# Kernel tuning notes

Measured on AMD Instinct MI355X. Metric: run time of the kernel, lower is better.

The kernel has to match this reference:

```python
import jax, jax.numpy as jnp
import numpy as np

NUM_HEAD = 2
KR = 3          # kernel_range = [3, 3]
SHIFT = 1
N_P = KR * KR   # 9 taps
PAD = (KR // 2) * SHIFT  # 1
OFFSETS = [(i, j) for i in (-(KR // 2), 0, KR // 2) if True for j in ()]  # placeholder, real list below
OFFSETS = [(i, j) for i in range(-(KR // 2), KR // 2 + 1) for j in range(-(KR // 2), KR // 2 + 1)]


def _conv3x3(x, w, b):
    # x: [B,H,W,Cin], w: [3,3,Cin,Cout] -> SAME conv + bias
    y = jax.lax.conv_general_dilated(
        x, w, window_strides=(1, 1), padding='SAME',
        dimension_numbers=('NHWC', 'HWIO', 'NHWC'))
    return y + b


def setup_inputs() -> dict:
    key = jax.random.key(0)
    B, H, W, D = 4, 128, 128, 64
    ks = jax.random.split(key, 10)
    sc = 0.05  # small init like glorot
    return {
        'x': jax.random.normal(ks[0], (B, H, W, D), jnp.float32),
        # 1x1 conv kernels stored as matrices (equiv. to (1,1,Cin,Cout))
        'K_P': jax.random.normal(ks[1], (D, D * N_P), jnp.float32) * sc,
        'V_P': jax.random.normal(ks[2], (D, D * N_P), jnp.float32) * sc,
        'Q_P': jax.random.normal(ks[3], (D, D), jnp.float32) * sc,
        'ff1_kernel': jax.random.normal(ks[4], (D, D), jnp.float32) * sc,
        'ff1_bias': jax.random.normal(ks[5], (D,), jnp.float32) * sc,
        'ff2_kernel': jax.random.normal(ks[6], (3, 3, D, 2 * D), jnp.float32) * sc,
        'ff2_bias': jax.random.normal(ks[7], (2 * D,), jnp.float32) * sc,
        'ff3_kernel': jax.random.normal(ks[8], (3, 3, 2 * D, D), jnp.float32) * sc,
        'ff3_bias': jax.random.normal(ks[9], (D,), jnp.float32) * sc,
    }


def reference(x, K_P, V_P, Q_P, ff1_kernel, ff1_bias, ff2_kernel, ff2_bias,
              ff3_kernel, ff3_bias):
    B, H, W, D = x.shape
    hd = D // NUM_HEAD

    # 1x1 projections; K/V produce N_P channel chunks, one per tap
    x_k = jnp.einsum('bhwd,de->bhwe', x, K_P).reshape(B, H, W, N_P, D)
    x_v = jnp.einsum('bhwd,de->bhwe', x, V_P).reshape(B, H, W, N_P, D)
    x_q = jnp.einsum('bhwd,de->bhwe', x, Q_P)

    pad5 = ((0, 0), (PAD, PAD), (PAD, PAD), (0, 0), (0, 0))
    k_pad = jnp.pad(x_k, pad5)
    v_pad = jnp.pad(x_v, pad5)

    # tap t uses channel chunk t at spatial offset OFFSETS[t]*SHIFT
    def taps(padded):
        return jnp.stack(
            [padded[:, PAD + i * SHIFT:PAD + i * SHIFT + H,
                    PAD + j * SHIFT:PAD + j * SHIFT + W, t, :]
             for t, (i, j) in enumerate(OFFSETS)], axis=3)  # [B,H,W,N_P,D]

    k_taps = taps(k_pad)
    v_taps = taps(v_pad)

    # validity mask (padded taps get score 0 before softmax, as in original)
    m_pad = jnp.pad(jnp.ones((B, H, W), x.dtype), ((0, 0), (PAD, PAD), (PAD, PAD)))
    mask = jnp.stack(
        [m_pad[:, PAD + i * SHIFT:PAD + i * SHIFT + H,
               PAD + j * SHIFT:PAD + j * SHIFT + W]
         for (i, j) in OFFSETS], axis=3)  # [B,H,W,N_P]

    kh = k_taps.reshape(B, H, W, N_P, NUM_HEAD, hd)
    vh = v_taps.reshape(B, H, W, N_P, NUM_HEAD, hd)
    qh = x_q.reshape(B, H, W, NUM_HEAD, hd)

    # scores per head over taps; masked-multiply then /3, as in original
    scores = jnp.einsum('bhwtnc,bhwnc->bhwnt', kh, qh)
    scores = scores * mask[:, :, :, None, :] / 3.0
    alpha = jax.nn.softmax(scores, axis=-1)  # over taps
    attn = jnp.einsum('bhwnt,bhwtnc->bhwnc', alpha, vh).reshape(B, H, W, D)

    # FFN: 1x1 conv -> relu -> 3x3 conv -> relu -> 3x3 conv -> relu
    t = jax.nn.relu(jnp.einsum('bhwd,de->bhwe', attn, ff1_kernel) + ff1_bias)
    t = jax.nn.relu(_conv3x3(t, ff2_kernel, ff2_bias))
    t = jax.nn.relu(_conv3x3(t, ff3_kernel, ff3_bias))
    return t
```

## Files before the change

### kernel.cpp

```cpp
#include <hip/hip_runtime.h>


typedef _Float16 half8 __attribute__((ext_vector_type(8)));
typedef float f32x4 __attribute__((ext_vector_type(4)));

#define PLANE 524288

__device__ __forceinline__ f32x4 mfma16(half8 a, half8 b, f32x4 c) {
  return __builtin_amdgcn_mfma_f32_16x16x32_f16(a, b, c, 0, 0, 0);
}
__device__ __forceinline__ half8 ldfrag(const _Float16* p) { return *(const half8*)p; }
__device__ __forceinline__ half8 zfrag() { half8 z = {}; return z; }

__device__ __forceinline__ void gload_lds16(const _Float16* g, _Float16* l) {
  __builtin_amdgcn_global_load_lds(
      (const __attribute__((address_space(1))) void*)g,
      (__attribute__((address_space(3))) void*)l, 16, 0, 0);
}

__global__ __launch_bounds__(256) void prep(
    const float* __restrict__ x, const float* __restrict__ Kp,
    const float* __restrict__ Vp, const float* __restrict__ Qp,
    const float* __restrict__ W1, const float* __restrict__ F2,
    const float* __restrict__ F3, _Float16* __restrict__ xh,
    _Float16* __restrict__ out) {
  if (blockIdx.x < 2048) {
    const int t = threadIdx.x;
    const int px = blockIdx.x * 32 + (t >> 3);
    const int oct = t & 7;
    const float4* s = (const float4*)(x + (size_t)px * 64 + oct * 8);
    float4 a = s[0], b = s[1];
    half8 h = { (_Float16)a.x, (_Float16)a.y, (_Float16)a.z, (_Float16)a.w,
                (_Float16)b.x, (_Float16)b.y, (_Float16)b.z, (_Float16)b.w };
    *(half8*)(xh + (size_t)oct * PLANE + (size_t)px * 8) = h;
    return;
  }
  int e = (blockIdx.x - 2048) * 256 + threadIdx.x;
  int j = e & 7, l = (e >> 3) & 63, f = e >> 9;
  int l15 = l & 15, q8 = (l >> 4) * 8;
  float v;
  if (f < 8)        { int mb = f >> 1, kb = f & 1;
                      v = Qp[(kb*32 + q8 + j) * 64 + mb*16 + l15]; }
  else if (f < 80)  { int g = f - 8, t = g >> 3, mb = (g >> 1) & 3, kb = g & 1;
                      v = Kp[(kb*32 + q8 + j) * 576 + t*64 + mb*16 + l15]; }
  else if (f < 152) { int g = f - 80, t = g >> 3, kb = (g >> 2) & 1, nb = g & 3;
                      v = Vp[(kb*32 + q8 + j) * 576 + t*64 + nb*16 + l15]; }
  else if (f < 160) { int g = f - 152, kb = g >> 2, nb = g & 3;
                      v = W1[(kb*32 + q8 + j) * 64 + nb*16 + l15]; }
  else if (f < 304) { int g = f - 160, t = g >> 4, kb = (g >> 3) & 1, nb = g & 7;
                      v = F2[(t*64 + kb*32 + q8 + j) * 128 + nb*16 + l15]; }
  else              { int g = f - 304, t = g >> 4, kb = (g >> 2) & 3, nb = g & 3;
                      v = F3[(t*128 + kb*32 + q8 + j) * 64 + nb*16 + l15]; }
  out[e] = (_Float16)v;
}

__global__ __launch_bounds__(512) void attn_ff1(
    const _Float16* __restrict__ xh, const _Float16* __restrict__ wf,
    const float* __restrict__ f1b, _Float16* __restrict__ t1g) {
  extern __shared__ _Float16 smem[];
  const int lane = threadIdx.x & 63, wid = threadIdx.x >> 6;
  const int l15 = lane & 15, q8 = (lane >> 4) * 8;
  const int row = blockIdx.x * 2 + (wid >> 2);
  const int rw = wid & 3;
  const int p0 = row * 128 + rw * 32;
  const int h = row & 127;
  const int w0 = rw * 32;
  const int oct0 = lane >> 4;
  float* dent = (float*)(smem + 77824) + wid * 64;

  {
    const _Float16* gw = wf + 4096 + (size_t)(wid * 19) * 512;
    _Float16* lw = smem + wid * 19 * 512;
    for (int i = 0; i < 19; ++i)
      gload_lds16(gw + i * 512 + lane * 8, lw + i * 512);
  }

  half8 ax0[2], ax1[2];
#pragma unroll
  for (int m = 0; m < 2; ++m) {
    const size_t px = (size_t)(p0 + m * 16 + l15);
    ax0[m] = ldfrag(xh + (size_t)oct0 * PLANE + px * 8);
    ax1[m] = ldfrag(xh + (size_t)(oct0 + 4) * PLANE + px * 8);
  }
  f32x4 qT[2][4];
#pragma unroll
  for (int cb = 0; cb < 4; ++cb) {
    half8 aq0 = ldfrag(wf + (cb * 2 + 0) * 512 + lane * 8);
    half8 aq1 = ldfrag(wf + (cb * 2 + 1) * 512 + lane * 8);
#pragma unroll
    for (int m = 0; m < 2; ++m) {
      f32x4 c = {};
      c = mfma16(aq0, ax0[m], c);
      c = mfma16(aq1, ax1[m], c);
      qT[m][cb] = c;
    }
  }

  auto load_tap = [&](int t, half8 (&x0)[2], half8 (&x1)[2]) {
    const int dh = t / 3 - 1, dw = t % 3 - 1;
    const bool rk = (unsigned)(h + dh) < 128u;
#pragma unroll
    for (int m = 0; m < 2; ++m) {
      const bool cv = rk && ((unsigned)(w0 + m * 16 + l15 + dw) < 128u);
      const size_t px = (size_t)(p0 + m * 16 + l15 + dh * 128 + dw);
      x0[m] = cv ? ldfrag(xh + (size_t)oct0 * PLANE + px * 8) : zfrag();
      x1[m] = cv ? ldfrag(xh + (size_t)(oct0 + 4) * PLANE + px * 8) : zfrag();
    }
  };

  float den0[2] = {0.f, 0.f}, den1[2] = {0.f, 0.f};
  auto score_tap = [&](int t, half8 (&x0)[2], half8 (&x1)[2],
                       float (&e0)[2], float (&e1)[2]) {
    const int dh = t / 3 - 1;
    const bool rowok = (unsigned)(h + dh) < 128u;
    half8 kf[8];
    if (rowok) {
#pragma unroll
      for (int f = 0; f < 8; ++f)
        kf[f] = ldfrag(smem + (t * 8 + f) * 512 + lane * 8);
    }
#pragma unroll
    for (int m = 0; m < 2; ++m) {
      float pa = 0.f, pb = 0.f;
      if (rowok) {
#pragma unroll
        for (int cb = 0; cb < 4; ++cb) {
          f32x4 c = {};
          c = mfma16(kf[cb * 2 + 0], x0[m], c);
          c = mfma16(kf[cb * 2 + 1], x1[m], c);
          float d = qT[m][cb].x * c.x + qT[m][cb].y * c.y
                  + qT[m][cb].z * c.z + qT[m][cb].w * c.w;
          if (cb < 2) pa += d; else pb += d;
        }
        pa += __shfl_xor(pa, 16, 64); pa += __shfl_xor(pa, 32, 64);
        pb += __shfl_xor(pb, 16, 64); pb += __shfl_xor(pb, 32, 64);
      }
      e0[m] = __expf(pa * (1.f / 3.f));
      e1[m] = __expf(pb * (1.f / 3.f));
      den0[m] += e0[m]; den1[m] += e1[m];
    }
  };

  half8 sx0[2], sx1[2];
  load_tap(0, sx0, sx1);

  __syncthreads();

  float e0c[2], e1c[2];
  score_tap(0, sx0, sx1, e0c, e1c);

  const _Float16* BVl = smem + 36864;
  f32x4 at[2][4];
#pragma unroll
  for (int m = 0; m < 2; ++m)
#pragma unroll
    for (int nb = 0; nb < 4; ++nb) at[m][nb] = f32x4{};

#pragma unroll
  for (int t = 0; t < 9; ++t) {
    const bool rowok = (unsigned)(h + (t / 3 - 1)) < 128u;
    half8 nx0[2], nx1[2];
    if (t < 8) load_tap(t + 1, nx0, nx1);
    if (rowok) {
      half8 vf[8];
#pragma unroll
      for (int f = 0; f < 8; ++f) vf[f] = ldfrag(BVl + (t * 8 + f) * 512 + lane * 8);
#pragma unroll
      for (int m = 0; m < 2; ++m) {
        _Float16 h0 = (_Float16)e0c[m], h1 = (_Float16)e1c[m];
        half8 b0 = {h0, h0, h0, h0, h0, h0, h0, h0};
        half8 b1 = {h1, h1, h1, h1, h1, h1, h1, h1};
        half8 s00 = sx0[m] * b0, s01 = sx1[m] * b0;
        half8 s10 = sx0[m] * b1, s11 = sx1[m] * b1;
#pragma unroll
        for (int nb = 0; nb < 2; ++nb) {
          at[m][nb]     = mfma16(s00, vf[0 * 4 + nb],     at[m][nb]);
          at[m][nb]     = mfma16(s01, vf[1 * 4 + nb],     at[m][nb]);
          at[m][nb + 2] = mfma16(s10, vf[0 * 4 + nb + 2], at[m][nb + 2]);
          at[m][nb + 2] = mfma16(s11, vf[1 * 4 + nb + 2], at[m][nb + 2]);
        }
      }
    }
    if (t < 8) {
      float e0n[2], e1n[2];
      score_tap(t + 1, nx0, nx1, e0n, e1n);
#pragma unroll
      for (int m = 0; m < 2; ++m) {
        sx0[m] = nx0[m]; sx1[m] = nx1[m];
        e0c[m] = e0n[m]; e1c[m] = e1n[m];
      }
    }
  }

#pragma unroll
  for (int m = 0; m < 2; ++m) {
    dent[(m * 2 + 0) * 16 + l15] = den0[m];
    dent[(m * 2 + 1) * 16 + l15] = den1[m];
  }
  f32x4 iv[2][2];
#pragma unroll
  for (int m = 0; m < 2; ++m)
#pragma unroll
    for (int hd = 0; hd < 2; ++hd) {
      f32x4 dv = *(const f32x4*)(dent + (m * 2 + hd) * 16 + (lane >> 4) * 4);
      iv[m][hd] = f32x4{1.f / dv.x, 1.f / dv.y, 1.f / dv.z, 1.f / dv.w};
    }

  __syncthreads();
  _Float16* myt = smem + wid * 2304;
#pragma unroll
  for (int m = 0; m < 2; ++m)
#pragma unroll
    for (int nb = 0; nb < 4; ++nb) {
      const int hd = nb >> 1;
#pragma unroll
      for (int r = 0; r < 4; ++r)
        myt[m * 1152 + ((lane >> 4) * 4 + r) * 72 + nb * 16 + l15] =
            (_Float16)(at[m][nb][r] * iv[m][hd][r]);
    }
  const _Float16* B1l = smem + 73728;
#pragma unroll
  for (int m = 0; m < 2; ++m) {
    half8 aa0 = ldfrag(myt + m * 1152 + l15 * 72 + q8);
    half8 aa1 = ldfrag(myt + m * 1152 + l15 * 72 + 32 + q8);
#pragma unroll
    for (int nb = 0; nb < 4; ++nb) {
      f32x4 c = {};
      c = mfma16(aa0, ldfrag(B1l + (0 * 4 + nb) * 512 + lane * 8), c);
      c = mfma16(aa1, ldfrag(B1l + (1 * 4 + nb) * 512 + lane * 8), c);
      float bv = f1b[nb * 16 + l15];
      const int ch = nb * 16 + l15;
      const size_t pbase = (size_t)(ch >> 3) * PLANE + (ch & 7);
#pragma unroll
      for (int r = 0; r < 4; ++r) {
        float v = fmaxf(c[r] + bv, 0.f);
        size_t px = (size_t)(p0 + m * 16 + (lane >> 4) * 4 + r);
        t1g[pbase + px * 8] = (_Float16)v;
      }
    }
  }
}

template <int KB, int NBL, int COUT>
__global__ __launch_bounds__(512, 2) void conv3x3(
    const _Float16* __restrict__ in, const _Float16* __restrict__ wfrag,
    const float* __restrict__ bias, void* __restrict__ outp, int out_fp32) {
  extern __shared__ _Float16 smem[];
  const int lane = threadIdx.x & 63, wid = threadIdx.x >> 6;
  const int l15 = lane & 15;
  const int nh = blockIdx.x & 1;
  const int pairIdx = blockIdx.x >> 1;
  const int row = pairIdx * 2 + (wid >> 2);
  const int rw = wid & 3;
  const int p0 = row * 128 + rw * 32;
  const int h = row & 127;
  const int w0 = rw * 32;
  const int NBF = COUT / 16;
  const int oct0 = lane >> 4;

  {
    for (int s = 0; s < 9; ++s) {
      int f = wid * 9 + s;
      int t = f >> 3, r = f & 7, kb = r / NBL, i = r % NBL;
      const _Float16* g = wfrag + (size_t)((t * KB + kb) * NBF + nh * NBL + i) * 512;
      gload_lds16(g + lane * 8, smem + f * 512);
    }
  }

  f32x4 acc[2][NBL];
#pragma unroll
  for (int m = 0; m < 2; ++m)
#pragma unroll
    for (int nb = 0; nb < NBL; ++nb) acc[m][nb] = f32x4{};

  half8 a[2][KB];
  {
    const bool rk = (unsigned)(h - 1) < 128u;
#pragma unroll
    for (int m = 0; m < 2; ++m) {
      const bool cv = rk && ((unsigned)(w0 + m * 16 + l15 - 1) < 128u);
      const size_t px = (size_t)(p0 + m * 16 + l15 - 129);
#pragma unroll
      for (int kb = 0; kb < KB; ++kb)
        a[m][kb] = cv ? ldfrag(in + (size_t)(kb * 4 + oct0) * PLANE + px * 8) : zfrag();
    }
  }

  __syncthreads();

#pragma unroll
  for (int t = 0; t < 9; ++t) {
    const int dh = t / 3 - 1;
    const bool rowok = (unsigned)(h + dh) < 128u;
    half8 an[2][KB];
    if (t < 8) {
      const int dh2 = (t + 1) / 3 - 1, dw2 = (t + 1) % 3 - 1;
      const bool rk2 = (unsigned)(h + dh2) < 128u;
#pragma unroll
      for (int m = 0; m < 2; ++m) {
        const bool cv = rk2 && ((unsigned)(w0 + m * 16 + l15 + dw2) < 128u);
        const size_t px = (size_t)(p0 + m * 16 + l15 + dh2 * 128 + dw2);
#pragma unroll
        for (int kb = 0; kb < KB; ++kb)
          an[m][kb] = cv ? ldfrag(in + (size_t)(kb * 4 + oct0) * PLANE + px * 8) : zfrag();
      }
    }
    if (rowok) {
#pragma unroll
      for (int nb = 0; nb < NBL; ++nb) {
#pragma unroll
        for (int kb = 0; kb < KB; ++kb) {
          half8 b = ldfrag(smem + (size_t)((t * KB + kb) * NBL + nb) * 512 + lane * 8);
          acc[0][nb] = mfma16(a[0][kb], b, acc[0][nb]);
          acc[1][nb] = mfma16(a[1][kb], b, acc[1][nb]);
        }
      }
    }
    if (t < 8) {
#pragma unroll
      for (int m = 0; m < 2; ++m)
#pragma unroll
        for (int kb = 0; kb < KB; ++kb) a[m][kb] = an[m][kb];
    }
  }

#pragma unroll
  for (int m = 0; m < 2; ++m)
#pragma unroll
    for (int nb = 0; nb < NBL; ++nb) {
      const int ch = nh * NBL * 16 + nb * 16 + l15;
      float bv = bias[ch];
#pragma unroll
      for (int r = 0; r < 4; ++r) {
        float v = fmaxf(acc[m][nb][r] + bv, 0.f);
        size_t px = (size_t)(p0 + m * 16 + (lane >> 4) * 4 + r);
        if (out_fp32) {
          ((float*)outp)[px * COUT + ch] = v;
        } else {
          ((_Float16*)outp)[(size_t)(ch >> 3) * PLANE + px * 8 + (ch & 7)] = (_Float16)v;
        }
      }
    }
}

extern "C" void kernel_launch(void* const* d_in, const int* in_sizes, int n_in,
                              void* d_out, int out_size, void* d_ws, size_t ws_size,
                              hipStream_t stream) {
  (void)in_sizes; (void)n_in; (void)out_size; (void)ws_size;
  const float* x   = (const float*)d_in[0];
  const float* Kp  = (const float*)d_in[1];
  const float* Vp  = (const float*)d_in[2];
  const float* Qp  = (const float*)d_in[3];
  const float* f1w = (const float*)d_in[4];
  const float* f1b = (const float*)d_in[5];
  const float* f2w = (const float*)d_in[6];
  const float* f2b = (const float*)d_in[7];
  const float* f3w = (const float*)d_in[8];
  const float* f3b = (const float*)d_in[9];

  _Float16* xh  = (_Float16*)d_ws;
  _Float16* wf  = xh + 4194304;
  _Float16* t1g = wf + 229376;
  _Float16* t2g = t1g + 4194304;
  float* outp = (float*)d_out;

  (void)hipFuncSetAttribute((const void*)attn_ff1,
      hipFuncAttributeMaxDynamicSharedMemorySize, 157696);
  (void)hipFuncSetAttribute((const void*)conv3x3<2, 4, 128>,
      hipFuncAttributeMaxDynamicSharedMemorySize, 73728);
  (void)hipFuncSetAttribute((const void*)conv3x3<4, 2, 64>,
      hipFuncAttributeMaxDynamicSharedMemorySize, 73728);

  prep<<<2944, 256, 0, stream>>>(x, Kp, Vp, Qp, f1w, f2w, f3w, xh, wf);
  attn_ff1<<<256, 512, 157696, stream>>>(xh, wf, f1b, t1g);
  conv3x3<2, 4, 128><<<512, 512, 73728, stream>>>(t1g, wf + 81920, f2b, t2g, 0);
  conv3x3<4, 2, 64><<<512, 512, 73728, stream>>>(t2g, wf + 155648, f3b, outp, 1);
}
```

Measured before the change: 145.3 us.

## Read weight fragments directly from global memory instead of staging in LDS

Removes the global-to-LDS staging of the K, V, FF1 and conv weight fragments in all three compute kernels and drops the associated barriers. The MFMA B operands are now loaded straight from global memory, relying on L1/L2 caching. Dynamic shared memory shrinks from about 154 KB to 38 KB for attn_ff1 and to zero for the convs, and launch bounds ask for 4 blocks per CU. This is meant to raise occupancy and cut barrier and staging latency, at the cost of repeated global or cache loads of the same weights by every wave and a tighter register budget.

```diff
diff --git a/kernel.cpp b/kernel.cpp
--- a/kernel.cpp
+++ b/kernel.cpp
@@ -11,12 +11,6 @@
 }
 __device__ __forceinline__ half8 ldfrag(const _Float16* p) { return *(const half8*)p; }
 __device__ __forceinline__ half8 zfrag() { half8 z = {}; return z; }
-
-__device__ __forceinline__ void gload_lds16(const _Float16* g, _Float16* l) {
-  __builtin_amdgcn_global_load_lds(
-      (const __attribute__((address_space(1))) void*)g,
-      (__attribute__((address_space(3))) void*)l, 16, 0, 0);
-}
 
 __global__ __launch_bounds__(256) void prep(
     const float* __restrict__ x, const float* __restrict__ Kp,
@@ -54,7 +48,7 @@
   out[e] = (_Float16)v;
 }
 
-__global__ __launch_bounds__(512) void attn_ff1(
+__global__ __launch_bounds__(512, 4) void attn_ff1(
     const _Float16* __restrict__ xh, const _Float16* __restrict__ wf,
     const float* __restrict__ f1b, _Float16* __restrict__ t1g) {
   extern __shared__ _Float16 smem[];
@@ -66,14 +60,11 @@
   const int h = row & 127;
   const int w0 = rw * 32;
   const int oct0 = lane >> 4;
-  float* dent = (float*)(smem + 77824) + wid * 64;
-
-  {
-    const _Float16* gw = wf + 4096 + (size_t)(wid * 19) * 512;
-    _Float16* lw = smem + wid * 19 * 512;
-    for (int i = 0; i < 19; ++i)
-      gload_lds16(gw + i * 512 + lane * 8, lw + i * 512);
-  }
+  const _Float16* AK = wf + 4096;
+  const _Float16* BV = wf + 40960;
+  const _Float16* B1 = wf + 77824;
+  _Float16* myt = smem + wid * 2304;
+  float* dent = (float*)(smem + 18432) + wid * 64;
 
   half8 ax0[2], ax1[2];
 #pragma unroll
@@ -117,7 +108,7 @@
     if (rowok) {
 #pragma unroll
       for (int f = 0; f < 8; ++f)
-        kf[f] = ldfrag(smem + (t * 8 + f) * 512 + lane * 8);
+        kf[f] = ldfrag(AK + (size_t)(t * 8 + f) * 512 + lane * 8);
     }
 #pragma unroll
     for (int m = 0; m < 2; ++m) {
@@ -144,12 +135,9 @@
   half8 sx0[2], sx1[2];
   load_tap(0, sx0, sx1);
 
-  __syncthreads();
-
   float e0c[2], e1c[2];
   score_tap(0, sx0, sx1, e0c, e1c);
 
-  const _Float16* BVl = smem + 36864;
   f32x4 at[2][4];
 #pragma unroll
   for (int m = 0; m < 2; ++m)
@@ -164,7 +152,8 @@
     if (rowok) {
       half8 vf[8];
 #pragma unroll
-      for (int f = 0; f < 8; ++f) vf[f] = ldfrag(BVl + (t * 8 + f) * 512 + lane * 8);
+      for (int f = 0; f < 8; ++f)
+        vf[f] = ldfrag(BV + (size_t)(t * 8 + f) * 512 + lane * 8);
 #pragma unroll
       for (int m = 0; m < 2; ++m) {
         _Float16 h0 = (_Float16)e0c[m], h1 = (_Float16)e1c[m];
@@ -206,8 +195,6 @@
       iv[m][hd] = f32x4{1.f / dv.x, 1.f / dv.y, 1.f / dv.z, 1.f / dv.w};
     }
 
-  __syncthreads();
-  _Float16* myt = smem + wid * 2304;
 #pragma unroll
   for (int m = 0; m < 2; ++m)
 #pragma unroll
@@ -218,7 +205,6 @@
         myt[m * 1152 + ((lane >> 4) * 4 + r) * 72 + nb * 16 + l15] =
             (_Float16)(at[m][nb][r] * iv[m][hd][r]);
     }
-  const _Float16* B1l = smem + 73728;
 #pragma unroll
   for (int m = 0; m < 2; ++m) {
     half8 aa0 = ldfrag(myt + m * 1152 + l15 * 72 + q8);
@@ -226,8 +212,8 @@
 #pragma unroll
     for (int nb = 0; nb < 4; ++nb) {
       f32x4 c = {};
-      c = mfma16(aa0, ldfrag(B1l + (0 * 4 + nb) * 512 + lane * 8), c);
-      c = mfma16(aa1, ldfrag(B1l + (1 * 4 + nb) * 512 + lane * 8), c);
+      c = mfma16(aa0, ldfrag(B1 + (0 * 4 + nb) * 512 + lane * 8), c);
+      c = mfma16(aa1, ldfrag(B1 + (1 * 4 + nb) * 512 + lane * 8), c);
       float bv = f1b[nb * 16 + l15];
       const int ch = nb * 16 + l15;
       const size_t pbase = (size_t)(ch >> 3) * PLANE + (ch & 7);
@@ -242,10 +228,9 @@
 }
 
 template <int KB, int NBL, int COUT>
-__global__ __launch_bounds__(512, 2) void conv3x3(
+__global__ __launch_bounds__(512, 4) void conv3x3(
     const _Float16* __restrict__ in, const _Float16* __restrict__ wfrag,
     const float* __restrict__ bias, void* __restrict__ outp, int out_fp32) {
-  extern __shared__ _Float16 smem[];
   const int lane = threadIdx.x & 63, wid = threadIdx.x >> 6;
   const int l15 = lane & 15;
   const int nh = blockIdx.x & 1;
@@ -258,15 +243,6 @@
   const int NBF = COUT / 16;
   const int oct0 = lane >> 4;
 
-  {
-    for (int s = 0; s < 9; ++s) {
-      int f = wid * 9 + s;
-      int t = f >> 3, r = f & 7, kb = r / NBL, i = r % NBL;
-      const _Float16* g = wfrag + (size_t)((t * KB + kb) * NBF + nh * NBL + i) * 512;
-      gload_lds16(g + lane * 8, smem + f * 512);
-    }
-  }
-
   f32x4 acc[2][NBL];
 #pragma unroll
   for (int m = 0; m < 2; ++m)
@@ -285,8 +261,6 @@
         a[m][kb] = cv ? ldfrag(in + (size_t)(kb * 4 + oct0) * PLANE + px * 8) : zfrag();
     }
   }
-
-  __syncthreads();
 
 #pragma unroll
   for (int t = 0; t < 9; ++t) {
@@ -310,7 +284,8 @@
       for (int nb = 0; nb < NBL; ++nb) {
 #pragma unroll
         for (int kb = 0; kb < KB; ++kb) {
-          half8 b = ldfrag(smem + (size_t)((t * KB + kb) * NBL + nb) * 512 + lane * 8);
+          half8 b = ldfrag(wfrag + (size_t)((t * KB + kb) * NBF + nh * NBL + nb) * 512
+                           + lane * 8);
           acc[0][nb] = mfma16(a[0][kb], b, acc[0][nb]);
           acc[1][nb] = mfma16(a[1][kb], b, acc[1][nb]);
         }
@@ -364,15 +339,8 @@
   _Float16* t2g = t1g + 4194304;
   float* outp = (float*)d_out;
 
-  (void)hipFuncSetAttribute((const void*)attn_ff1,
-      hipFuncAttributeMaxDynamicSharedMemorySize, 157696);
-  (void)hipFuncSetAttribute((const void*)conv3x3<2, 4, 128>,
-      hipFuncAttributeMaxDynamicSharedMemorySize, 73728);
-  (void)hipFuncSetAttribute((const void*)conv3x3<4, 2, 64>,
-      hipFuncAttributeMaxDynamicSharedMemorySize, 73728);
-
   prep<<<2944, 256, 0, stream>>>(x, Kp, Vp, Qp, f1w, f2w, f3w, xh, wf);
-  attn_ff1<<<256, 512, 157696, stream>>>(xh, wf, f1b, t1g);
-  conv3x3<2, 4, 128><<<512, 512, 73728, stream>>>(t1g, wf + 81920, f2b, t2g, 0);
-  conv3x3<4, 2, 64><<<512, 512, 73728, stream>>>(t2g, wf + 155648, f3b, outp, 1);
-}
+  attn_ff1<<<256, 512, 38912, stream>>>(xh, wf, f1b, t1g);
+  conv3x3<2, 4, 128><<<512, 512, 0, stream>>>(t1g, wf + 81920, f2b, t2g, 0);
+  conv3x3<4, 2, 64><<<512, 512, 0, stream>>>(t2g, wf + 155648, f3b, outp, 1);
+}
```

New measurement: 183.8 us. 1.27x slower.
